# Optimization experiments

Measured on AMD Instinct MI355X. Metric: run time of the kernel, lower is better.

The kernel has to match this reference:

```python
import jax, jax.numpy as jnp
import numpy as np

ALPHA = 0.3

def setup_inputs() -> dict:
    key = jax.random.key(0)
    k1, k2, k3, k4 = jax.random.split(key, 4)
    bz, sl, n_pos = 64, 1024, 50
    a_arc = jax.random.normal(k1, (bz, sl, sl), dtype=jnp.float32)
    s_arc = jax.random.normal(k2, (bz, sl, sl), dtype=jnp.float32)
    adds = jax.random.randint(k3, (bz, sl), 0, n_pos, dtype=jnp.int32)
    pos = jax.random.randint(k4, (bz, sl), 0, n_pos, dtype=jnp.int32)
    return {"a_arc": a_arc, "s_arc": s_arc, "adds": adds, "pos": pos, "n_pos": n_pos}


def reference(a_arc, s_arc, adds, pos, n_pos):
    # Bin index for every (head, dep) pair: bin = adds[b,i]*n_pos + adds[b,j]
    bins_add = adds[:, :, None] * n_pos + adds[:, None, :]          # [bz, sl, sl] int32
    # Histogram: sum a_arc values per POS-pair bin (replaces the O(n_pos^2) masked loop)
    score_arc = jax.ops.segment_sum(
        a_arc.reshape(-1), bins_add.reshape(-1), num_segments=n_pos * n_pos)
    score_arc = jax.nn.sigmoid(score_arc)                            # [n_pos^2]
    # Broadcast the binned scores back onto s_arc via the pos-pair bins
    bins_pos = pos[:, :, None] * n_pos + pos[:, None, :]             # [bz, sl, sl]
    return s_arc + ALPHA * score_arc[bins_pos]
```

## Files before the change

### kernel.cpp

```cpp
#include <hip/hip_runtime.h>

constexpr int NPOS  = 50;
constexpr int NBINS = NPOS * NPOS;
constexpr int SL    = 1024;
constexpr int BZ    = 64;
constexpr float ALPHA = 0.3f;
constexpr int NSLICE = 4;

using f32x4  = __attribute__((ext_vector_type(4))) float;
using bf16x8 = __attribute__((ext_vector_type(8))) short;

constexpr int H_THREADS = 256;
constexpr int H_ROWS    = 64;
constexpr int KSPLIT    = 2;
constexpr int KSTEPS    = (SL / KSPLIT) / 32;
constexpr int H_BLOCKS  = BZ * (SL / H_ROWS) * KSPLIT;

constexpr int A_THREADS      = 256;
constexpr int ROWS_PER_BLOCK = 32;
constexpr int BLOCKS_PER_B   = SL / ROWS_PER_BLOCK;
constexpr int A_BLOCKS       = BZ * BLOCKS_PER_B;

__global__ __launch_bounds__(H_THREADS) void hist_mfma(
    const float* __restrict__ a, const int* __restrict__ adds,
    float* __restrict__ g_hist) {
  __shared__ int   adds_s[SL];
  __shared__ float T_lds[H_ROWS][66];
  __shared__ float acc2[NPOS * 52];
  __shared__ int   orderR[H_ROWS];
  __shared__ int   cntR[NPOS], offm[NPOS];

  const int tid   = threadIdx.x;
  const int b     = blockIdx.x >> 5;
  const int rem   = blockIdx.x & 31;
  const int rblk  = rem >> 1;
  const int khalf = rem & 1;
  const int row0  = rblk * H_ROWS;
  const int j0b   = khalf * (SL / KSPLIT);

  ((int4*)adds_s)[tid] = ((const int4*)(adds + (size_t)b * SL))[tid];
  for (int k = tid; k < NPOS * 52; k += H_THREADS) acc2[k] = 0.0f;
  if (tid < NPOS) cntR[tid] = 0;
  __syncthreads();

  if (tid < H_ROWS) atomicAdd(&cntR[adds_s[row0 + tid]], 1);
  __syncthreads();
  if (tid == 0) {
    int run = 0;
    for (int c = 0; c < NPOS; ++c) { offm[c] = run; run += cntR[c]; }
  }
  __syncthreads();
  if (tid < H_ROWS)
    orderR[atomicAdd(&offm[adds_s[row0 + tid]], 1)] = tid;

  const int wid = tid >> 6, lane = tid & 63;
  const int kg = lane >> 4, l15 = lane & 15;
  const float* __restrict__ Arow =
      a + ((size_t)b * SL + row0 + wid * 16 + l15) * SL + j0b + kg * 8;

  struct PF { float4 va, vb; int4 w0, w1; };
  auto loadpf = [&](PF& buf, int ks) {
    const float* p_ = Arow + ks * 32;
    buf.va = ((const float4*)p_)[0];
    buf.vb = ((const float4*)p_)[1];
    const int kkl = j0b + ks * 32 + kg * 8;
    buf.w0 = *(const int4*)&adds_s[kkl];
    buf.w1 = *(const int4*)&adds_s[kkl + 4];
  };

  f32x4 acc[4] = {};
  auto compute = [&](const PF& buf) {
    const float f[8] = {buf.va.x, buf.va.y, buf.va.z, buf.va.w,
                        buf.vb.x, buf.vb.y, buf.vb.z, buf.vb.w};
    const int av[8] = {buf.w0.x, buf.w0.y, buf.w0.z, buf.w0.w,
                       buf.w1.x, buf.w1.y, buf.w1.z, buf.w1.w};
    bf16x8 ah, al;
    #pragma unroll
    for (int e = 0; e < 8; ++e) {
      const unsigned u = __builtin_bit_cast(unsigned, f[e]);
      ah[e] = (short)(u >> 16);
      const float hf = __builtin_bit_cast(float, u & 0xFFFF0000u);
      const float lo = f[e] - hf;
      al[e] = (short)(__builtin_bit_cast(unsigned, lo) >> 16);
    }
    #pragma unroll
    for (int qt = 0; qt < 4; ++qt) {
      const int q = qt * 16 + l15;
      bf16x8 bq;
      #pragma unroll
      for (int e = 0; e < 8; ++e)
        bq[e] = (av[e] == q) ? (short)0x3F80 : (short)0;
      acc[qt] = __builtin_amdgcn_mfma_f32_16x16x32_bf16(ah, bq, acc[qt], 0, 0, 0);
      acc[qt] = __builtin_amdgcn_mfma_f32_16x16x32_bf16(al, bq, acc[qt], 0, 0, 0);
    }
  };

  PF pfA, pfB;
  loadpf(pfA, 0);
  for (int ks = 0; ks < KSTEPS; ks += 2) {
    loadpf(pfB, ks + 1);
    compute(pfA);
    if (ks + 2 < KSTEPS) loadpf(pfA, ks + 2);
    compute(pfB);
  }

  #pragma unroll
  for (int qt = 0; qt < 4; ++qt)
    #pragma unroll
    for (int r = 0; r < 4; ++r)
      T_lds[wid * 16 + kg * 4 + r][qt * 16 + l15] = acc[qt][r];
  __syncthreads();

  {
    const int q = tid & 63, quarter = tid >> 6;
    float s = 0.0f;
    int pcur = -1;
    for (int k2 = 0; k2 < H_ROWS / 4; ++k2) {
      const int row = orderR[quarter * (H_ROWS / 4) + k2];
      const int p   = adds_s[row0 + row];
      if (p != pcur) {
        if (pcur >= 0 && q < NPOS) atomicAdd(&acc2[pcur * 52 + q], s);
        pcur = p; s = 0.0f;
      }
      s += T_lds[row][q];
    }
    if (pcur >= 0 && q < NPOS) atomicAdd(&acc2[pcur * 52 + q], s);
  }
  __syncthreads();

  float* __restrict__ gs = g_hist + (size_t)(blockIdx.x & (NSLICE - 1)) * NBINS;
  for (int bin = tid; bin < NBINS; bin += H_THREADS) {
    const float v = acc2[(bin / NPOS) * 52 + (bin % NPOS)];
    if (v != 0.0f) atomicAdd(&gs[bin], v);
  }
}

__global__ __launch_bounds__(A_THREADS) void apply_kernel(
    const float* __restrict__ s, const int* __restrict__ pos,
    const float* __restrict__ g_hist, float* __restrict__ out) {
  __shared__ float sig[NBINS];
  __shared__ int   pos_s[SL];

  const int tid = threadIdx.x;
  const int b   = blockIdx.x / BLOCKS_PER_B;
  const int i0  = (blockIdx.x % BLOCKS_PER_B) * ROWS_PER_BLOCK;

  ((int4*)pos_s)[tid] = ((const int4*)(pos + (size_t)b * SL))[tid];
  for (int k = tid; k < NBINS; k += A_THREADS) {
    const float h = g_hist[k] + g_hist[NBINS + k] +
                    g_hist[2 * NBINS + k] + g_hist[3 * NBINS + k];
    sig[k] = 1.0f / (1.0f + __expf(-h));
  }
  __syncthreads();

  const int4 pj = ((const int4*)pos_s)[tid];
  const size_t rowoff = ((size_t)b * SL + i0) * SL;
  const float4* __restrict__ srow = (const float4*)(s + rowoff);
  float4* __restrict__ orow = (float4*)(out + rowoff);

  for (int r = 0; r < ROWS_PER_BLOCK; ++r) {
    const int base = pos_s[i0 + r] * NPOS;
    const float4 sv = srow[(size_t)r * (SL / 4) + tid];
    float4 ov;
    ov.x = sv.x + ALPHA * sig[base + pj.x];
    ov.y = sv.y + ALPHA * sig[base + pj.y];
    ov.z = sv.z + ALPHA * sig[base + pj.z];
    ov.w = sv.w + ALPHA * sig[base + pj.w];
    orow[(size_t)r * (SL / 4) + tid] = ov;
  }
}

extern "C" void kernel_launch(void* const* d_in, const int* in_sizes, int n_in,
                              void* d_out, int out_size, void* d_ws, size_t ws_size,
                              hipStream_t stream) {
  const float* a_arc = (const float*)d_in[0];
  const float* s_arc = (const float*)d_in[1];
  const int*   adds  = (const int*)d_in[2];
  const int*   pos   = (const int*)d_in[3];
  float* out    = (float*)d_out;
  float* g_hist = (float*)d_ws;

  hipMemsetAsync(g_hist, 0, NSLICE * NBINS * sizeof(float), stream);

  hist_mfma   <<<H_BLOCKS, H_THREADS, 0, stream>>>(a_arc, adds, g_hist);
  apply_kernel<<<A_BLOCKS, A_THREADS, 0, stream>>>(s_arc, pos, g_hist, out);
}
```

Before: 190.5 us.

## Replace global histogram atomics with per-block partials and a reduction kernel

Each histogram block now writes its full 2500-bin partial to its own workspace slice instead of issuing atomicAdds into four shared slices. A new reduce kernel sums the 2048 partials per bin (in 16 groups, then 16 atomics per bin) into a single histogram read by the apply kernel. This removes heavy global atomic contention but adds about 20 MB of partial writes and reads plus an extra kernel launch.

```diff
diff --git a/kernel.cpp b/kernel.cpp
--- a/kernel.cpp
+++ b/kernel.cpp
@@ -5,7 +5,6 @@
 constexpr int SL    = 1024;
 constexpr int BZ    = 64;
 constexpr float ALPHA = 0.3f;
-constexpr int NSLICE = 4;
 
 using f32x4  = __attribute__((ext_vector_type(4))) float;
 using bf16x8 = __attribute__((ext_vector_type(8))) short;
@@ -15,6 +14,12 @@
 constexpr int KSPLIT    = 2;
 constexpr int KSTEPS    = (SL / KSPLIT) / 32;
 constexpr int H_BLOCKS  = BZ * (SL / H_ROWS) * KSPLIT;
+constexpr int PSTRIDE   = 2560;
+
+constexpr int R_THREADS = 256;
+constexpr int R_BINGRP  = 40;
+constexpr int R_PGRP    = 16;
+constexpr int R_BLOCKS  = R_BINGRP * R_PGRP;
 
 constexpr int A_THREADS      = 256;
 constexpr int ROWS_PER_BLOCK = 32;
@@ -23,7 +28,7 @@
 
 __global__ __launch_bounds__(H_THREADS) void hist_mfma(
     const float* __restrict__ a, const int* __restrict__ adds,
-    float* __restrict__ g_hist) {
+    float* __restrict__ g_part) {
   __shared__ int   adds_s[SL];
   __shared__ float T_lds[H_ROWS][66];
   __shared__ float acc2[NPOS * 52];
@@ -128,11 +133,29 @@
   }
   __syncthreads();
 
-  float* __restrict__ gs = g_hist + (size_t)(blockIdx.x & (NSLICE - 1)) * NBINS;
-  for (int bin = tid; bin < NBINS; bin += H_THREADS) {
-    const float v = acc2[(bin / NPOS) * 52 + (bin % NPOS)];
-    if (v != 0.0f) atomicAdd(&gs[bin], v);
-  }
+  float* __restrict__ gp = g_part + (size_t)blockIdx.x * PSTRIDE;
+  for (int bin = tid; bin < NBINS; bin += H_THREADS)
+    gp[bin] = acc2[(bin / NPOS) * 52 + (bin % NPOS)];
+}
+
+__global__ __launch_bounds__(R_THREADS) void reduce_kernel(
+    const float* __restrict__ g_part, float* __restrict__ g_hist) {
+  __shared__ float red[4][64];
+  const int bx  = blockIdx.x % R_BINGRP;
+  const int py  = blockIdx.x / R_BINGRP;
+  const int w   = threadIdx.x >> 6, l = threadIdx.x & 63;
+  const int bin = bx * 64 + l;
+
+  float s = 0.0f;
+  if (bin < NBINS) {
+    const float* base = g_part + ((size_t)py * 128 + w * 32) * PSTRIDE + bin;
+    #pragma unroll
+    for (int r = 0; r < 32; ++r) s += base[(size_t)r * PSTRIDE];
+  }
+  red[w][l] = s;
+  __syncthreads();
+  if (w == 0 && bin < NBINS)
+    atomicAdd(&g_hist[bin], red[0][l] + red[1][l] + red[2][l] + red[3][l]);
 }
 
 __global__ __launch_bounds__(A_THREADS) void apply_kernel(
@@ -147,8 +170,7 @@
 
   ((int4*)pos_s)[tid] = ((const int4*)(pos + (size_t)b * SL))[tid];
   for (int k = tid; k < NBINS; k += A_THREADS) {
-    const float h = g_hist[k] + g_hist[NBINS + k] +
-                    g_hist[2 * NBINS + k] + g_hist[3 * NBINS + k];
+    const float h = g_hist[k];
     sig[k] = 1.0f / (1.0f + __expf(-h));
   }
   __syncthreads();
@@ -179,9 +201,11 @@
   const int*   pos   = (const int*)d_in[3];
   float* out    = (float*)d_out;
   float* g_hist = (float*)d_ws;
-
-  hipMemsetAsync(g_hist, 0, NSLICE * NBINS * sizeof(float), stream);
-
-  hist_mfma   <<<H_BLOCKS, H_THREADS, 0, stream>>>(a_arc, adds, g_hist);
-  apply_kernel<<<A_BLOCKS, A_THREADS, 0, stream>>>(s_arc, pos, g_hist, out);
-}
+  float* g_part = g_hist + 4096;
+
+  hipMemsetAsync(g_hist, 0, NBINS * sizeof(float), stream);
+
+  hist_mfma    <<<H_BLOCKS, H_THREADS, 0, stream>>>(a_arc, adds, g_part);
+  reduce_kernel<<<R_BLOCKS, R_THREADS, 0, stream>>>(g_part, g_hist);
+  apply_kernel <<<A_BLOCKS, A_THREADS, 0, stream>>>(s_arc, pos, g_hist, out);
+}
```

Measured after the change: 196.4 us. 1.03x slower.
